# Performance work log

Measured on AMD Instinct MI355X. Metric: run time of the kernel, lower is better.

Reference implementation:

```python
import jax, jax.numpy as jnp
import numpy as np

B, D, H, K = 32768, 64, 512, 8
P = 3 * K - 1            # widths(K) + heights(K) + interior derivatives(K-1)
BOUND = 4.0
MIN_BIN = 1e-3           # min bin width/height fraction
MIN_DERIV = 1e-3


def setup_inputs() -> dict:
    key = jax.random.key(0)
    k0, k1, k2, k3 = jax.random.split(key, 4)
    x = jax.random.normal(k0, (B, D), jnp.float32) * 2.0
    W1 = jax.random.normal(k1, (H, D), jnp.float32) / np.sqrt(D)
    b1 = jnp.zeros((H,), jnp.float32)
    W2 = jax.random.normal(k2, (D * P, H), jnp.float32) / np.sqrt(H)
    b2 = jax.random.normal(k3, (D * P,), jnp.float32) * 0.01
    m_in = np.arange(1, D + 1)                      # input degrees 1..D
    m_hid = (np.arange(H) % (D - 1)) + 1            # hidden degrees 1..D-1
    M1 = jnp.asarray((m_hid[:, None] >= m_in[None, :]).astype(np.float32))   # [H, D]
    m_out = (np.arange(D * P) // P) + 1             # output degree = dim index + 1
    M2 = jnp.asarray((m_out[:, None] > m_hid[None, :]).astype(np.float32))   # [D*P, H]
    return {"x": x, "W1": W1, "b1": b1, "W2": W2, "b2": b2, "M1": M1, "M2": M2}


def _rqs(x, w_un, h_un, d_un):
    """Monotonic rational-quadratic spline (elementwise over [B, D]).
    w_un, h_un: [B, D, K] unnormalized widths/heights; d_un: [B, D, K-1].
    Returns (y [B, D], logabsdet [B, D])."""
    f32 = x.dtype
    w = jax.nn.softmax(w_un, axis=-1)
    hh = jax.nn.softmax(h_un, axis=-1)
    w = MIN_BIN + (1.0 - MIN_BIN * K) * w
    hh = MIN_BIN + (1.0 - MIN_BIN * K) * hh
    edge_lo = jnp.full(w.shape[:-1] + (1,), -BOUND, f32)
    edge_hi = jnp.full(w.shape[:-1] + (1,), BOUND, f32)
    # knot positions [B, D, K+1] with exact endpoints at +-BOUND
    xk = jnp.concatenate([edge_lo, -BOUND + 2.0 * BOUND * jnp.cumsum(w, -1)[..., :-1], edge_hi], -1)
    yk = jnp.concatenate([edge_lo, -BOUND + 2.0 * BOUND * jnp.cumsum(hh, -1)[..., :-1], edge_hi], -1)
    widths = xk[..., 1:] - xk[..., :-1]
    heights = yk[..., 1:] - yk[..., :-1]
    ones = jnp.ones(w.shape[:-1] + (1,), f32)
    # boundary derivatives fixed to 1 (identity outside the box)
    d = jnp.concatenate([ones, MIN_DERIV + jax.nn.softplus(d_un), ones], -1)  # [B, D, K+1]

    inside = (x >= -BOUND) & (x <= BOUND)
    xc = jnp.clip(x, -BOUND, BOUND)
    # bucketize: index of containing bin
    idx = jnp.clip(jnp.sum((xc[..., None] >= xk).astype(jnp.int32), -1) - 1, 0, K - 1)

    def g(a, off=0):
        return jnp.take_along_axis(a, idx[..., None] + off, axis=-1)[..., 0]

    x_k, y_k = g(xk), g(yk)
    w_k, h_k = g(widths), g(heights)
    d_k, d_k1 = g(d), g(d, 1)
    s = h_k / w_k
    theta = (xc - x_k) / w_k
    t1m = theta * (1.0 - theta)
    num = h_k * (s * theta * theta + d_k * t1m)
    den = s + (d_k1 + d_k - 2.0 * s) * t1m
    y_in = y_k + num / den
    dnum = s * s * (d_k1 * theta * theta + 2.0 * s * t1m + d_k * (1.0 - theta) ** 2)
    ld_in = jnp.log(dnum) - 2.0 * jnp.log(den)
    y = jnp.where(inside, y_in, x)
    ld = jnp.where(inside, ld_in, 0.0)
    return y, ld


def _forward(x, W1, b1, W2, b2, M1, M2):
    hmid = jax.nn.relu(x @ (W1 * M1).T + b1)          # [B, H]
    params = (hmid @ (W2 * M2).T + b2).reshape(x.shape[0], D, P)
    w_un = params[..., :K]
    h_un = params[..., K:2 * K]
    d_un = params[..., 2 * K:]
    z, ld = _rqs(x, w_un, h_un, d_un)
    return z, jnp.sum(ld, axis=-1)                    # logDet per example


def reference(x, W1, b1, W2, b2, M1, M2):
    return _forward(x, W1, b1, W2, b2, M1, M2)
```

## Files before the change

### kernel.cpp

```cpp
#include <hip/hip_runtime.h>
#include <math.h>

#define NB    32768
#define DDIM  64
#define HDIM  512
#define PDIM  23
#define KBINS 8
#define BM    32
#define NCOLS (DDIM * PDIM)
#define CHUNK 368
#define PSTRIDE 372
#define NTILES 92

#define RQ_BOUND  4.0f
#define RQ_MINBIN 0.001f
#define RQ_MINDER 0.001f

typedef __attribute__((ext_vector_type(8))) _Float16 half8;
typedef __attribute__((ext_vector_type(4))) float f32x4;
typedef unsigned short ushort_t;

__global__ __launch_bounds__(256) void prep_frag(const float* __restrict__ W1,
                                                 const float* __restrict__ W2,
                                                 _Float16* __restrict__ W1g,
                                                 _Float16* __restrict__ W2g) {
    const int gid = blockIdx.x * 256 + threadIdx.x;
    const int NW1 = 32 * 2 * 64;
    if (gid < NW1) {
        const int lane = gid & 63;
        const int tk   = gid >> 6;
        const int kt   = tk & 1, ht = tk >> 1;
        const int h = ht * 16 + (lane & 15);
        const int k = kt * 32 + (lane >> 4) * 8;
        const float* src = W1 + h * DDIM + k;
        const int hm63 = h % 63;
        half8 v;
        #pragma unroll
        for (int e = 0; e < 8; ++e)
            v[e] = (_Float16)(((k + e) <= hm63) ? src[e] : 0.0f);
        *(half8*)(W1g + (size_t)gid * 8) = v;
    } else {
        const int g2 = gid - NW1;
        if (g2 < NTILES * 16 * 64) {
            const int lane = g2 & 63;
            const int tk   = g2 >> 6;
            const int kt   = tk & 15, T = tk >> 4;
            const int col  = T * 16 + (lane & 15);
            const int k    = kt * 32 + (lane >> 4) * 8;
            const float* src = W2 + (size_t)col * HDIM + k;
            const int d = col / PDIM;
            half8 v;
            #pragma unroll
            for (int e = 0; e < 8; ++e)
                v[e] = (_Float16)((d > ((k + e) % 63)) ? src[e] : 0.0f);
            *(half8*)(W2g + (size_t)g2 * 8) = v;
        }
    }
}

__device__ __forceinline__ float fexp(float v)  { return __expf(v); }
__device__ __forceinline__ float flog(float v)  { return __logf(v); }
__device__ __forceinline__ float fdiv(float a, float b) { return __fdividef(a, b); }

__global__ __launch_bounds__(512, 4) void fused_flow(
    const float* __restrict__ x,  const float* __restrict__ b1,
    const float* __restrict__ b2, const _Float16* __restrict__ W1g,
    const _Float16* __restrict__ W2g,
    float* __restrict__ z_out, float* __restrict__ ld_out)
{
    __shared__ __align__(16) ushort_t hm[BM * 512];
    __shared__ __align__(16) float pstage[BM * PSTRIDE];

    const int t    = threadIdx.x;
    const int row0 = blockIdx.x * BM;
    const int wv   = t >> 6;
    const int lane = t & 63;
    const int l15  = lane & 15;
    const int lg   = lane >> 4;

    char* hmB = (char*)hm;

    {
        f32x4 acc1[4][2];
        #pragma unroll
        for (int j = 0; j < 4; ++j)
            #pragma unroll
            for (int m = 0; m < 2; ++m) acc1[j][m] = (f32x4){0.f, 0.f, 0.f, 0.f};

        #pragma unroll
        for (int kt = 0; kt < 2; ++kt) {
            half8 a[2];
            #pragma unroll
            for (int m = 0; m < 2; ++m) {
                const float* xr = x + (size_t)(row0 + m * 16 + l15) * DDIM + kt * 32 + lg * 8;
                const float4 xa = *(const float4*)(xr);
                const float4 xb = *(const float4*)(xr + 4);
                a[m][0] = (_Float16)xa.x; a[m][1] = (_Float16)xa.y;
                a[m][2] = (_Float16)xa.z; a[m][3] = (_Float16)xa.w;
                a[m][4] = (_Float16)xb.x; a[m][5] = (_Float16)xb.y;
                a[m][6] = (_Float16)xb.z; a[m][7] = (_Float16)xb.w;
            }
            #pragma unroll
            for (int j = 0; j < 4; ++j) {
                const half8 b = *(const half8*)(W1g + (size_t)(wv * 4 + j) * 1024 + kt * 512 + lane * 8);
                #pragma unroll
                for (int m = 0; m < 2; ++m)
                    acc1[j][m] = __builtin_amdgcn_mfma_f32_16x16x32_f16(a[m], b, acc1[j][m], 0, 0, 0);
            }
        }
        #pragma unroll
        for (int j = 0; j < 4; ++j) {
            const int h = (wv * 4 + j) * 16 + l15;
            const float bias = b1[h];
            #pragma unroll
            for (int m = 0; m < 2; ++m) {
                #pragma unroll
                for (int q = 0; q < 4; ++q) {
                    const int r = m * 16 + lg * 4 + q;
                    const _Float16 hv = (_Float16)fmaxf(acc1[j][m][q] + bias, 0.0f);
                    *(ushort_t*)(hmB + r * 1024 + ((h * 2) ^ ((r & 7) << 4))) =
                        __builtin_bit_cast(ushort_t, hv);
                }
            }
        }
    }
    __syncthreads();

    float ldacc = 0.0f;
    const int srow = t >> 4;
    const int sd   = t & 15;
    const int tbase = wv * 3;
    const float CNORM = 1.0f - RQ_MINBIN * KBINS;

    const _Float16* w2base[3];
    #pragma unroll
    for (int i = 0; i < 3; ++i) {
        const int tile = (tbase + i < 23) ? (tbase + i) : 22;
        w2base[i] = W2g + (size_t)tile * 8192 + lane * 8;
    }

    f32x4 acc[3][2];
    float xk[KBINS + 1], yk[KBINS + 1], dv[KBINS + 1];

#define ZERO_ACC                                                            \
    _Pragma("unroll")                                                       \
    for (int i = 0; i < 3; ++i)                                             \
        _Pragma("unroll")                                                   \
        for (int m = 0; m < 2; ++m) acc[i][m] = (f32x4){0.f, 0.f, 0.f, 0.f};

#define KTG(CN, K0)                                                         \
    {                                                                       \
        const size_t coff = (size_t)(CN) * (23 * 8192);                     \
        _Pragma("unroll")                                                   \
        for (int kt = (K0); kt < (K0) + 4; ++kt) {                          \
            half8 ah[2];                                                    \
            _Pragma("unroll")                                               \
            for (int m = 0; m < 2; ++m) {                                   \
                const int r  = m * 16 + l15;                                \
                const int kb = (kt * 32 + lg * 8) * 2;                      \
                ah[m] = *(const half8*)(hmB + r * 1024 + (kb ^ ((r & 7) << 4))); \
            }                                                               \
            half8 bfr[3];                                                   \
            _Pragma("unroll")                                               \
            for (int i = 0; i < 3; ++i)                                     \
                bfr[i] = *(const half8*)(w2base[i] + coff + kt * 512);      \
            _Pragma("unroll")                                               \
            for (int i = 0; i < 3; ++i)                                     \
                _Pragma("unroll")                                           \
                for (int m = 0; m < 2; ++m)                                 \
                    acc[i][m] = __builtin_amdgcn_mfma_f32_16x16x32_f16(ah[m], bfr[i], acc[i][m], 0, 0, 0); \
        }                                                                   \
    }

#define STAGE(CN)                                                           \
    _Pragma("unroll")                                                       \
    for (int i = 0; i < 3; ++i) {                                           \
        if (tbase + i < 23) {                                               \
            const int lcol = (tbase + i) * 16 + l15;                        \
            _Pragma("unroll")                                               \
            for (int m = 0; m < 2; ++m)                                     \
                _Pragma("unroll")                                           \
                for (int q = 0; q < 4; ++q)                                 \
                    pstage[(m * 16 + lg * 4 + q) * PSTRIDE + lcol] = acc[i][m][q]; \
        }                                                                   \
    }

#define SPL_A(CS)                                                           \
    {                                                                       \
        const float* pp = &pstage[srow * PSTRIDE + sd * PDIM];              \
        const float* bp = b2 + (size_t)((CS) * 16 + sd) * PDIM;             \
        float e[8]; float s = 0.0f;                                         \
        _Pragma("unroll")                                                   \
        for (int i = 0; i < 8; ++i) { e[i] = fexp(pp[i] + bp[i]); s += e[i]; } \
        const float cinv = CNORM * fdiv(1.0f, s);                           \
        float cum = 0.0f;                                                   \
        xk[0] = -RQ_BOUND;                                                  \
        _Pragma("unroll")                                                   \
        for (int i = 0; i < 8; ++i) {                                       \
            cum += fmaf(e[i], cinv, RQ_MINBIN);                             \
            xk[i + 1] = fmaf(cum, 2.0f * RQ_BOUND, -RQ_BOUND);              \
        }                                                                   \
        xk[KBINS] = RQ_BOUND;                                               \
    }

#define SPL_B(CS)                                                           \
    {                                                                       \
        const float* pp = &pstage[srow * PSTRIDE + sd * PDIM];              \
        const float* bp = b2 + (size_t)((CS) * 16 + sd) * PDIM;             \
        float e[8]; float s = 0.0f;                                         \
        _Pragma("unroll")                                                   \
        for (int i = 0; i < 8; ++i) { e[i] = fexp(pp[8 + i] + bp[8 + i]); s += e[i]; } \
        const float cinv = CNORM * fdiv(1.0f, s);                           \
        float cum = 0.0f;                                                   \
        yk[0] = -RQ_BOUND;                                                  \
        _Pragma("unroll")                                                   \
        for (int i = 0; i < 8; ++i) {                                       \
            cum += fmaf(e[i], cinv, RQ_MINBIN);                             \
            yk[i + 1] = fmaf(cum, 2.0f * RQ_BOUND, -RQ_BOUND);              \
        }                                                                   \
        yk[KBINS] = RQ_BOUND;                                               \
    }

#define SPL_C(CS)                                                           \
    {                                                                       \
        const float* pp = &pstage[srow * PSTRIDE + sd * PDIM];              \
        const float* bp = b2 + (size_t)((CS) * 16 + sd) * PDIM;             \
        dv[0] = 1.0f;                                                       \
        _Pragma("unroll")                                                   \
        for (int i = 0; i < 7; ++i)                                         \
            dv[i + 1] = RQ_MINDER + flog(1.0f + fexp(pp[16 + i] + bp[16 + i])); \
        dv[KBINS] = 1.0f;                                                   \
    }

#define SPL_D(CS)                                                           \
    {                                                                       \
        const int dcol = (CS) * 16 + sd;                                    \
        const float xorig = x[(size_t)(row0 + srow) * DDIM + dcol];         \
        const float xc = fminf(fmaxf(xorig, -RQ_BOUND), RQ_BOUND);          \
        const bool inside = (xorig >= -RQ_BOUND) && (xorig <= RQ_BOUND);    \
        int idx = 0;                                                        \
        _Pragma("unroll")                                                   \
        for (int i = 1; i < KBINS; ++i) idx += (xc >= xk[i]) ? 1 : 0;       \
        float x_k = xk[0], x_k1 = xk[1];                                    \
        float y_k = yk[0], y_k1 = yk[1];                                    \
        float d_k = dv[0], d_k1 = dv[1];                                    \
        _Pragma("unroll")                                                   \
        for (int i = 1; i < KBINS; ++i) {                                   \
            const bool mm = (idx == i);                                     \
            x_k  = mm ? xk[i]     : x_k;                                    \
            x_k1 = mm ? xk[i + 1] : x_k1;                                   \
            y_k  = mm ? yk[i]     : y_k;                                    \
            y_k1 = mm ? yk[i + 1] : y_k1;                                   \
            d_k  = mm ? dv[i]     : d_k;                                    \
            d_k1 = mm ? dv[i + 1] : d_k1;                                   \
        }                                                                   \
        const float w_k = x_k1 - x_k;                                       \
        const float h_k = y_k1 - y_k;                                       \
        const float rw  = fdiv(1.0f, w_k);                                  \
        const float sv  = h_k * rw;                                         \
        const float th  = (xc - x_k) * rw;                                  \
        const float omt = 1.0f - th;                                        \
        const float t1m = th * omt;                                         \
        const float num = h_k * (sv * th * th + d_k * t1m);                 \
        const float den = sv + (d_k1 + d_k - 2.0f * sv) * t1m;              \
        const float yin = y_k + fdiv(num, den);                             \
        const float dnum = sv * sv * (d_k1 * th * th + 2.0f * sv * t1m + d_k * omt * omt); \
        const float ldin = flog(fdiv(dnum, den * den));                     \
        z_out[(size_t)(row0 + srow) * DDIM + dcol] = inside ? yin : xorig;  \
        ldacc += inside ? ldin : 0.0f;                                      \
    }

#define MERGED(CN, CS)                                                      \
    ZERO_ACC                                                                \
    KTG(CN, 0)  SPL_A(CS)                                                   \
    KTG(CN, 4)  SPL_B(CS)                                                   \
    KTG(CN, 8)  SPL_C(CS)                                                   \
    KTG(CN, 12) SPL_D(CS)

    ZERO_ACC
    KTG(0, 0) KTG(0, 4) KTG(0, 8) KTG(0, 12)
    STAGE(0)
    __syncthreads();

    MERGED(1, 0)
    __syncthreads();
    STAGE(1)
    __syncthreads();

    MERGED(2, 1)
    __syncthreads();
    STAGE(2)
    __syncthreads();

    MERGED(3, 2)
    __syncthreads();
    STAGE(3)
    __syncthreads();

    SPL_A(3) SPL_B(3) SPL_C(3) SPL_D(3)

#undef MERGED
#undef SPL_D
#undef SPL_C
#undef SPL_B
#undef SPL_A
#undef STAGE
#undef KTG
#undef ZERO_ACC

    ldacc += __shfl_xor(ldacc, 1, 64);
    ldacc += __shfl_xor(ldacc, 2, 64);
    ldacc += __shfl_xor(ldacc, 4, 64);
    ldacc += __shfl_xor(ldacc, 8, 64);
    if (sd == 0) ld_out[row0 + srow] = ldacc;
}

extern "C" void kernel_launch(void* const* d_in, const int* in_sizes, int n_in,
                              void* d_out, int out_size, void* d_ws, size_t ws_size,
                              hipStream_t stream) {
    (void)in_sizes; (void)n_in; (void)out_size; (void)ws_size;
    const float* x  = (const float*)d_in[0];
    const float* W1 = (const float*)d_in[1];
    const float* b1 = (const float*)d_in[2];
    const float* W2 = (const float*)d_in[3];
    const float* b2 = (const float*)d_in[4];

    _Float16* W1g = (_Float16*)d_ws;
    _Float16* W2g = W1g + HDIM * DDIM;
    float* z  = (float*)d_out;
    float* ld = z + (size_t)NB * DDIM;

    const int n_groups = 32 * 2 * 64 + NTILES * 16 * 64;
    prep_frag<<<(n_groups + 255) / 256, 256, 0, stream>>>(W1, W2, W1g, W2g);
    fused_flow<<<NB / BM, 512, 0, stream>>>(x, b1, b2, W1g, W2g, z, ld);
}
```

Baseline: 90.47 us.

## Double row tile to 64 with 1024-thread blocks for more W2 reuse

Increases rows per block from 32 to 64 and block size to 1024 threads, remapping waves so each wave computes 4 row-tiles for one or two column tiles instead of 2 row-tiles for three. Each W2 fragment loaded from global memory now feeds twice as many MFMAs, cutting weight traffic per row. In exchange, LDS use roughly doubles (limiting residency to one block per CU), column-tile work is unevenly split across waves, and the grid has fewer blocks.

```diff
diff --git a/kernel.cpp b/kernel.cpp
--- a/kernel.cpp
+++ b/kernel.cpp
@@ -6,7 +6,7 @@
 #define HDIM  512
 #define PDIM  23
 #define KBINS 8
-#define BM    32
+#define BM    64
 #define NCOLS (DDIM * PDIM)
 #define CHUNK 368
 #define PSTRIDE 372
@@ -62,7 +62,7 @@
 __device__ __forceinline__ float flog(float v)  { return __logf(v); }
 __device__ __forceinline__ float fdiv(float a, float b) { return __fdividef(a, b); }
 
-__global__ __launch_bounds__(512, 4) void fused_flow(
+__global__ __launch_bounds__(1024, 4) void fused_flow(
     const float* __restrict__ x,  const float* __restrict__ b1,
     const float* __restrict__ b2, const _Float16* __restrict__ W1g,
     const _Float16* __restrict__ W2g,
@@ -81,17 +81,17 @@
     char* hmB = (char*)hm;
 
     {
-        f32x4 acc1[4][2];
+        f32x4 acc1[2][4];
         #pragma unroll
-        for (int j = 0; j < 4; ++j)
-            #pragma unroll
-            for (int m = 0; m < 2; ++m) acc1[j][m] = (f32x4){0.f, 0.f, 0.f, 0.f};
+        for (int j = 0; j < 2; ++j)
+            #pragma unroll
+            for (int m = 0; m < 4; ++m) acc1[j][m] = (f32x4){0.f, 0.f, 0.f, 0.f};
 
         #pragma unroll
         for (int kt = 0; kt < 2; ++kt) {
-            half8 a[2];
-            #pragma unroll
-            for (int m = 0; m < 2; ++m) {
+            half8 a[4];
+            #pragma unroll
+            for (int m = 0; m < 4; ++m) {
                 const float* xr = x + (size_t)(row0 + m * 16 + l15) * DDIM + kt * 32 + lg * 8;
                 const float4 xa = *(const float4*)(xr);
                 const float4 xb = *(const float4*)(xr + 4);
@@ -101,19 +101,20 @@
                 a[m][6] = (_Float16)xb.z; a[m][7] = (_Float16)xb.w;
             }
             #pragma unroll
-            for (int j = 0; j < 4; ++j) {
-                const half8 b = *(const half8*)(W1g + (size_t)(wv * 4 + j) * 1024 + kt * 512 + lane * 8);
+            for (int j = 0; j < 2; ++j) {
+                const int ht = wv * 2 + j;
+                const half8 b = *(const half8*)(W1g + (size_t)ht * 1024 + kt * 512 + lane * 8);
                 #pragma unroll
-                for (int m = 0; m < 2; ++m)
+                for (int m = 0; m < 4; ++m)
                     acc1[j][m] = __builtin_amdgcn_mfma_f32_16x16x32_f16(a[m], b, acc1[j][m], 0, 0, 0);
             }
         }
         #pragma unroll
-        for (int j = 0; j < 4; ++j) {
-            const int h = (wv * 4 + j) * 16 + l15;
+        for (int j = 0; j < 2; ++j) {
+            const int h = (wv * 2 + j) * 16 + l15;
             const float bias = b1[h];
             #pragma unroll
-            for (int m = 0; m < 2; ++m) {
+            for (int m = 0; m < 4; ++m) {
                 #pragma unroll
                 for (int q = 0; q < 4; ++q) {
                     const int r = m * 16 + lg * 4 + q;
@@ -129,59 +130,62 @@
     float ldacc = 0.0f;
     const int srow = t >> 4;
     const int sd   = t & 15;
-    const int tbase = wv * 3;
+    const bool two = (wv < 7);
     const float CNORM = 1.0f - RQ_MINBIN * KBINS;
 
-    const _Float16* w2base[3];
-    #pragma unroll
-    for (int i = 0; i < 3; ++i) {
-        const int tile = (tbase + i < 23) ? (tbase + i) : 22;
-        w2base[i] = W2g + (size_t)tile * 8192 + lane * 8;
-    }
-
-    f32x4 acc[3][2];
+    const _Float16* w2base[2];
+    w2base[0] = W2g + (size_t)wv * 8192 + lane * 8;
+    w2base[1] = W2g + (size_t)(two ? 16 + wv : 22) * 8192 + lane * 8;
+
+    f32x4 acc[2][4];
     float xk[KBINS + 1], yk[KBINS + 1], dv[KBINS + 1];
 
 #define ZERO_ACC                                                            \
     _Pragma("unroll")                                                       \
-    for (int i = 0; i < 3; ++i)                                             \
-        _Pragma("unroll")                                                   \
-        for (int m = 0; m < 2; ++m) acc[i][m] = (f32x4){0.f, 0.f, 0.f, 0.f};
+    for (int i = 0; i < 2; ++i)                                             \
+        _Pragma("unroll")                                                   \
+        for (int m = 0; m < 4; ++m) acc[i][m] = (f32x4){0.f, 0.f, 0.f, 0.f};
 
 #define KTG(CN, K0)                                                         \
     {                                                                       \
         const size_t coff = (size_t)(CN) * (23 * 8192);                     \
         _Pragma("unroll")                                                   \
         for (int kt = (K0); kt < (K0) + 4; ++kt) {                          \
-            half8 ah[2];                                                    \
+            half8 ah[4];                                                    \
             _Pragma("unroll")                                               \
-            for (int m = 0; m < 2; ++m) {                                   \
+            for (int m = 0; m < 4; ++m) {                                   \
                 const int r  = m * 16 + l15;                                \
                 const int kb = (kt * 32 + lg * 8) * 2;                      \
                 ah[m] = *(const half8*)(hmB + r * 1024 + (kb ^ ((r & 7) << 4))); \
             }                                                               \
-            half8 bfr[3];                                                   \
+            const half8 b0 = *(const half8*)(w2base[0] + coff + kt * 512);  \
             _Pragma("unroll")                                               \
-            for (int i = 0; i < 3; ++i)                                     \
-                bfr[i] = *(const half8*)(w2base[i] + coff + kt * 512);      \
+            for (int m = 0; m < 4; ++m)                                     \
+                acc[0][m] = __builtin_amdgcn_mfma_f32_16x16x32_f16(ah[m], b0, acc[0][m], 0, 0, 0); \
+            if (two) {                                                      \
+                const half8 b1f = *(const half8*)(w2base[1] + coff + kt * 512); \
+                _Pragma("unroll")                                           \
+                for (int m = 0; m < 4; ++m)                                 \
+                    acc[1][m] = __builtin_amdgcn_mfma_f32_16x16x32_f16(ah[m], b1f, acc[1][m], 0, 0, 0); \
+            }                                                               \
+        }                                                                   \
+    }
+
+#define STAGE(CN)                                                           \
+    {                                                                       \
+        const int lc0 = wv * 16 + l15;                                      \
+        _Pragma("unroll")                                                   \
+        for (int m = 0; m < 4; ++m)                                         \
             _Pragma("unroll")                                               \
-            for (int i = 0; i < 3; ++i)                                     \
-                _Pragma("unroll")                                           \
-                for (int m = 0; m < 2; ++m)                                 \
-                    acc[i][m] = __builtin_amdgcn_mfma_f32_16x16x32_f16(ah[m], bfr[i], acc[i][m], 0, 0, 0); \
-        }                                                                   \
-    }
-
-#define STAGE(CN)                                                           \
-    _Pragma("unroll")                                                       \
-    for (int i = 0; i < 3; ++i) {                                           \
-        if (tbase + i < 23) {                                               \
-            const int lcol = (tbase + i) * 16 + l15;                        \
+            for (int q = 0; q < 4; ++q)                                     \
+                pstage[(m * 16 + lg * 4 + q) * PSTRIDE + lc0] = acc[0][m][q]; \
+        if (two) {                                                          \
+            const int lc1 = (16 + wv) * 16 + l15;                           \
             _Pragma("unroll")                                               \
-            for (int m = 0; m < 2; ++m)                                     \
+            for (int m = 0; m < 4; ++m)                                     \
                 _Pragma("unroll")                                           \
                 for (int q = 0; q < 4; ++q)                                 \
-                    pstage[(m * 16 + lg * 4 + q) * PSTRIDE + lcol] = acc[i][m][q]; \
+                    pstage[(m * 16 + lg * 4 + q) * PSTRIDE + lc1] = acc[1][m][q]; \
         }                                                                   \
     }
 
@@ -332,5 +336,5 @@
 
     const int n_groups = 32 * 2 * 64 + NTILES * 16 * 64;
     prep_frag<<<(n_groups + 255) / 256, 256, 0, stream>>>(W1, W2, W1g, W2g);
-    fused_flow<<<NB / BM, 512, 0, stream>>>(x, b1, b2, W1g, W2g, z, ld);
+    fused_flow<<<NB / BM, 1024, 0, stream>>>(x, b1, b2, W1g, W2g, z, ld);
 }
```

Result: slower. 127.0 us (+40.3%).
